# Performance work log

Measured on AMD Instinct MI355X. Metric: run time of the kernel, lower is better.

Reference implementation:

```python
import jax, jax.numpy as jnp
import numpy as np

# Module config (from init_kwargs): Occ3D-nuScenes volume
VOL_MIN = np.array([-40.0, -40.0, -1.0], dtype=np.float32)
VOXEL_SIZE = 0.4
GRID_SHAPE = (200, 200, 16)  # (vol_max - vol_min) / voxel_size
K = 6          # fixed per-gaussian window; covers radii <= 0.6m (bbox span <= 5 voxels)
N_GAUSS = 32768
N_DIMS = 16


def setup_inputs() -> dict:
    key = jax.random.key(0)
    k1, k2, k3, k4, k5 = jax.random.split(key, 5)
    # Means strictly inside the volume with 1m margin so bboxes stay in-grid.
    lo = jnp.array([-39.0, -39.0, 0.0], dtype=jnp.float32)
    hi = jnp.array([39.0, 39.0, 4.4], dtype=jnp.float32)
    means3d = jax.random.uniform(k1, (N_GAUSS, 3), minval=lo, maxval=hi, dtype=jnp.float32)
    # SPD covariances: Q diag(s) Q^T with eigenvalues in [0.01, 0.04]
    A = jax.random.normal(k2, (N_GAUSS, 3, 3), dtype=jnp.float32)
    Q, _ = jnp.linalg.qr(A)
    s = jax.random.uniform(k3, (N_GAUSS, 3), minval=0.01, maxval=0.04, dtype=jnp.float32)
    covs = jnp.einsum('nij,nj,nkj->nik', Q, s, Q)
    opacities = jax.random.uniform(k4, (N_GAUSS,), dtype=jnp.float32)
    features = jax.random.normal(k5, (N_GAUSS, N_DIMS), dtype=jnp.float32)
    return {"means3d": means3d, "covs": covs, "opacities": opacities, "features": features}


def reference(means3d, covs, opacities, features):
    N, D = features.shape
    dim_x, dim_y, dim_z = GRID_SHAPE
    total = dim_x * dim_y * dim_z
    vol_min = jnp.asarray(VOL_MIN)

    inv_covs = jnp.linalg.inv(covs)                                  # [N,3,3]
    radii = 3.0 * jnp.sqrt(jnp.diagonal(covs, axis1=-2, axis2=-1))   # [N,3]

    # Bounding box in voxel indices (trunc toward zero, like the triton .to(int32))
    s = (means3d - radii - vol_min) / VOXEL_SIZE
    e = (means3d + radii - vol_min) / VOXEL_SIZE
    start = jnp.maximum(0, s.astype(jnp.int32))                      # [N,3]
    end = jnp.minimum(jnp.array(GRID_SHAPE, jnp.int32), e.astype(jnp.int32) + 1)

    offs = jnp.arange(K, dtype=jnp.int32)
    ix = start[:, 0:1] + offs   # [N,K]
    iy = start[:, 1:2] + offs
    iz = start[:, 2:3] + offs
    mask = ((ix < end[:, 0:1])[:, :, None, None]
            & (iy < end[:, 1:2])[:, None, :, None]
            & (iz < end[:, 2:3])[:, None, None, :])                  # [N,K,K,K]

    # Voxel-corner minus mean offsets (matches kernel: x*vs + vol_min - m)
    px = ix.astype(means3d.dtype) * VOXEL_SIZE + vol_min[0] - means3d[:, 0:1]  # [N,K]
    py = iy.astype(means3d.dtype) * VOXEL_SIZE + vol_min[1] - means3d[:, 1:2]
    pz = iz.astype(means3d.dtype) * VOXEL_SIZE + vol_min[2] - means3d[:, 2:3]
    d = jnp.stack(jnp.broadcast_arrays(px[:, :, None, None],
                                       py[:, None, :, None],
                                       pz[:, None, None, :]), axis=-1)  # [N,K,K,K,3]

    mahal = jnp.einsum('nxyzi,nij,nxyzj->nxyz', d, inv_covs, d)      # [N,K,K,K]
    density = opacities[:, None, None, None] * jnp.exp(-0.5 * mahal)
    density = jnp.where(mask, density, 0.0)

    flat_idx = (ix[:, :, None, None] * (dim_y * dim_z)
                + iy[:, None, :, None] * dim_z
                + iz[:, None, None, :])                               # [N,K,K,K]
    idx = flat_idx.reshape(-1)

    grid_density = jnp.zeros((total,), density.dtype).at[idx].add(density.reshape(-1))

    contrib = density[..., None] * features[:, None, None, None, :]   # [N,K,K,K,D]
    grid_feats = jnp.zeros((total, D), density.dtype).at[:, -1].set(1e-5)
    grid_feats = grid_feats.at[idx].add(contrib.reshape(-1, D))
    grid_feats = grid_feats / jnp.clip(grid_density, 1e-6, None)[:, None]

    return grid_density.reshape(GRID_SHAPE), grid_feats.reshape(*GRID_SHAPE, D)
```

## Files before the change

### kernel.cpp

```cpp
#include <hip/hip_runtime.h>
#include <math.h>

constexpr int   GX = 200, GY = 200, GZ = 16;
constexpr int   TOTAL = GX * GY * GZ;
constexpr int   ND = 16;
constexpr int   KW = 6;
constexpr float VS = 0.4f;
constexpr float VMINX = -40.0f, VMINY = -40.0f, VMINZ = -1.0f;

constexpr int   TS = 4;
constexpr int   TX = 50, TY = 50, TZ = 4;
constexpr int   NT = TX * TY * TZ;
constexpr int   RS = 20;
constexpr int   CAP = 128;
constexpr int   BR  = 12;
constexpr float NHL2E = -0.72134752044448170f;


__device__ __forceinline__ unsigned bf16_rne(float x) {
    unsigned u = __float_as_uint(x);
    return (u + 0x7fffu + ((u >> 16) & 1u)) >> 16;
}

__global__ __launch_bounds__(256) void gv_prep(
    const float* __restrict__ means, const float* __restrict__ covs,
    const float* __restrict__ opac,  const float* __restrict__ feats,
    float* __restrict__ gdata, int* __restrict__ counts,
    int* __restrict__ entries, int n)
{
    int g = blockIdx.x * 256 + threadIdx.x;
    if (g >= n) return;
    const float* cv = covs + (size_t)g * 9;
    float a = cv[0], b = cv[1], c = cv[2], d = cv[4], e = cv[5], f = cv[8];
    float A = d * f - e * e;
    float B = c * e - b * f;
    float C = b * e - c * d;
    float invdet = 1.0f / (a * A + b * B + c * C);
    float mx = means[g * 3 + 0], my = means[g * 3 + 1], mz = means[g * 3 + 2];
    float rx = 3.0f * sqrtf(a), ry = 3.0f * sqrtf(d), rz = 3.0f * sqrtf(f);
    int sx = max(0, (int)((mx - rx - VMINX) / VS));
    int sy = max(0, (int)((my - ry - VMINY) / VS));
    int sz = max(0, (int)((mz - rz - VMINZ) / VS));
    int ex = min(GX, (int)((mx + rx - VMINX) / VS) + 1); ex = min(ex, sx + KW);
    int ey = min(GY, (int)((my + ry - VMINY) / VS) + 1); ey = min(ey, sy + KW);
    int ez = min(GZ, (int)((mz + rz - VMINZ) / VS) + 1); ez = min(ez, sz + KW);

    float rec[RS];
    rec[0] = mx; rec[1] = my; rec[2] = mz; rec[3] = opac[g];
    rec[4] = (A * invdet) * NHL2E;
    rec[5] = (B * invdet) * (2.0f * NHL2E);
    rec[6] = (C * invdet) * (2.0f * NHL2E);
    rec[7] = ((a * f - c * c) * invdet) * NHL2E;
    rec[8] = ((b * c - a * e) * invdet) * (2.0f * NHL2E);
    rec[9] = ((a * d - b * b) * invdet) * NHL2E;
    rec[10] = __int_as_float(sx | (sy << 8) | (sz << 16));
    rec[11] = __int_as_float(ex | (ey << 8) | (ez << 16));
    const float* fr = feats + (size_t)g * ND;
#pragma unroll
    for (int q = 0; q < 8; ++q) {
        unsigned lo = bf16_rne(fr[2 * q]);
        unsigned hi = bf16_rne(fr[2 * q + 1]);
        rec[12 + q] = __uint_as_float(lo | (hi << 16));
    }
    float4* dst = (float4*)(gdata + (size_t)g * RS);
#pragma unroll
    for (int q = 0; q < 5; ++q) dst[q] = ((const float4*)rec)[q];

    int tx0 = sx >> 2, tx1 = (ex - 1) >> 2;
    int ty0 = sy >> 2, ty1 = (ey - 1) >> 2;
    int tz0 = sz >> 2, tz1 = (ez - 1) >> 2;
    for (int tx = tx0; tx <= tx1; ++tx)
        for (int ty = ty0; ty <= ty1; ++ty)
            for (int tz = tz0; tz <= tz1; ++tz) {
                int tile = (tx * TY + ty) * TZ + tz;
                int slot = atomicAdd(&counts[tile], 1);
                if (slot < CAP) entries[(size_t)tile * CAP + slot] = g;
            }
}

__global__ __launch_bounds__(256) void gv_tile(
    const float* __restrict__ gdata, const int* __restrict__ counts,
    const int* __restrict__ entries, float* __restrict__ out)
{
    const int wv   = threadIdx.x >> 6;
    const int lane = threadIdx.x & 63;
    const int p    = blockIdx.x * 4 + wv;
    const int tz   = p % TZ;
    const int ty   = (p / TZ) % TY;
    const int tx   = p / (TZ * TY);

    __shared__ float sbuf[4][2][BR * RS];

    const int lz = lane & 3, ly = (lane >> 2) & 3, lx = lane >> 4;
    const int ix = tx * TS + lx, iy = ty * TS + ly, iz = tz * TS + lz;
    const float pxc = (float)ix * VS + VMINX;
    const float pyc = (float)iy * VS + VMINY;
    const float pzc = (float)iz * VS + VMINZ;

    float accd = 0.0f;
    float accf[ND];
#pragma unroll
    for (int c = 0; c < ND; ++c) accf[c] = 0.0f;
    accf[ND - 1] = 1e-5f;

    const int cnt = __builtin_amdgcn_readfirstlane(min(counts[p], CAP));
    const int* __restrict__ el = entries + (size_t)p * CAP;

    const int  rl = lane / 5;
    const int  fc = lane - rl * 5;
    const bool stager = lane < 60;
    const int  wslot = rl * RS + fc * 4;

    if (cnt > 0) {
        const int nb = (cnt + BR - 1) / BR;
        float* b0 = &sbuf[wv][0][0];
        float* b1 = &sbuf[wv][1][0];

        float4 vn; int idn2 = 0;
        if (stager) {
            int id0 = el[min(rl, cnt - 1)];
            float4 v0 = *(const float4*)(gdata + (size_t)id0 * RS + fc * 4);
            *(float4*)(b0 + wslot) = v0;
            int idn = el[min(BR + rl, cnt - 1)];
            vn = *(const float4*)(gdata + (size_t)idn * RS + fc * 4);
            idn2 = el[min(2 * BR + rl, cnt - 1)];
        }

        for (int b = 0; b < nb; ++b) {
            if (b + 1 < nb && stager) {
                float* dstb = ((b + 1) & 1) ? b1 : b0;
                *(float4*)(dstb + wslot) = vn;
                vn = *(const float4*)(gdata + (size_t)idn2 * RS + fc * 4);
                idn2 = el[min((b + 3) * BR + rl, cnt - 1)];
            }
            const float* rb = (b & 1) ? b1 : b0;
            const int rn = min(BR, cnt - b * BR);
            for (int r = 0; r < rn; ++r) {
                const float* rec = rb + r * RS;
                float4 c2 = *(const float4*)(rec + 8);
                int spk = __float_as_int(c2.z), epk = __float_as_int(c2.w);
                int sx = spk & 255, sy = (spk >> 8) & 255, sz = (spk >> 16) & 255;
                int ex = epk & 255, ey = (epk >> 8) & 255, ez = (epk >> 16) & 255;
                bool in = (ix >= sx) & (ix < ex)
                        & (iy >= sy) & (iy < ey)
                        & (iz >= sz) & (iz < ez);

                float4 c0 = *(const float4*)(rec);
                float4 c1 = *(const float4*)(rec + 4);
                float px = pxc - c0.x;
                float py = pyc - c0.y;
                float pz = pzc - c0.z;
                float q = c1.x * px * px + c1.w * py * py + c2.y * pz * pz
                        + c1.y * px * py + c1.z * px * pz + c2.x * py * pz;
                float dens = c0.w * __builtin_amdgcn_exp2f(q);
                dens = in ? dens : 0.0f;
                accd += dens;

                uint4 fA = *(const uint4*)(rec + 12);
                uint4 fB = *(const uint4*)(rec + 16);
#define BFLO(u) __uint_as_float((u) << 16)
#define BFHI(u) __uint_as_float((u) & 0xffff0000u)
                accf[0]  = fmaf(dens, BFLO(fA.x), accf[0]);
                accf[1]  = fmaf(dens, BFHI(fA.x), accf[1]);
                accf[2]  = fmaf(dens, BFLO(fA.y), accf[2]);
                accf[3]  = fmaf(dens, BFHI(fA.y), accf[3]);
                accf[4]  = fmaf(dens, BFLO(fA.z), accf[4]);
                accf[5]  = fmaf(dens, BFHI(fA.z), accf[5]);
                accf[6]  = fmaf(dens, BFLO(fA.w), accf[6]);
                accf[7]  = fmaf(dens, BFHI(fA.w), accf[7]);
                accf[8]  = fmaf(dens, BFLO(fB.x), accf[8]);
                accf[9]  = fmaf(dens, BFHI(fB.x), accf[9]);
                accf[10] = fmaf(dens, BFLO(fB.y), accf[10]);
                accf[11] = fmaf(dens, BFHI(fB.y), accf[11]);
                accf[12] = fmaf(dens, BFLO(fB.z), accf[12]);
                accf[13] = fmaf(dens, BFHI(fB.z), accf[13]);
                accf[14] = fmaf(dens, BFLO(fB.w), accf[14]);
                accf[15] = fmaf(dens, BFHI(fB.w), accf[15]);
#undef BFLO
#undef BFHI
            }
        }
    }

    const int flat = (ix * GY + iy) * GZ + iz;
    out[flat] = accd;
    float inv = 1.0f / fmaxf(accd, 1e-6f);
    float4* fo = (float4*)(out + TOTAL + (size_t)flat * ND);
#pragma unroll
    for (int q = 0; q < 4; ++q) {
        float4 w;
        w.x = accf[q * 4 + 0] * inv;
        w.y = accf[q * 4 + 1] * inv;
        w.z = accf[q * 4 + 2] * inv;
        w.w = accf[q * 4 + 3] * inv;
        fo[q] = w;
    }
}

extern "C" void kernel_launch(void* const* d_in, const int* in_sizes, int n_in,
                              void* d_out, int out_size, void* d_ws, size_t ws_size,
                              hipStream_t stream) {
    const float* means = (const float*)d_in[0];
    const float* covs  = (const float*)d_in[1];
    const float* opac  = (const float*)d_in[2];
    const float* feats = (const float*)d_in[3];
    float* out = (float*)d_out;
    const int n = in_sizes[2];

    float* gdata   = (float*)d_ws;
    int*   counts  = (int*)(gdata + (size_t)n * RS);
    int*   entries = counts + ((NT + 63) & ~63);

    hipMemsetAsync(counts, 0, NT * sizeof(int), stream);
    gv_prep<<<(n + 255) / 256, 256, 0, stream>>>(means, covs, opac, feats,
                                                 gdata, counts, entries, n);
    gv_tile<<<NT / 4, 256, 0, stream>>>(gdata, counts, entries, out);
}
```

Before: 106.4 us.

## Compact gaussian record to 64 bytes and drop counts memset

```diff
diff --git a/kernel.cpp b/kernel.cpp
--- a/kernel.cpp
+++ b/kernel.cpp
@@ -1,4 +1,5 @@
 #include <hip/hip_runtime.h>
+#include <hip/hip_fp16.h>
 #include <math.h>
 
 constexpr int   GX = 200, GY = 200, GZ = 16;
@@ -11,22 +12,31 @@
 constexpr int   TS = 4;
 constexpr int   TX = 50, TY = 50, TZ = 4;
 constexpr int   NT = TX * TY * TZ;
-constexpr int   RS = 20;
+constexpr int   RS = 16;
 constexpr int   CAP = 128;
-constexpr int   BR  = 12;
+constexpr int   BR  = 16;
 constexpr float NHL2E = -0.72134752044448170f;
 
+
+__device__ int g_counts[NT];
 
 __device__ __forceinline__ unsigned bf16_rne(float x) {
     unsigned u = __float_as_uint(x);
     return (u + 0x7fffu + ((u >> 16) & 1u)) >> 16;
 }
+__device__ __forceinline__ float pk2bf(float a, float b) {
+    return __uint_as_float(bf16_rne(a) | (bf16_rne(b) << 16));
+}
+__device__ __forceinline__ float pk2h(float a, float b) {
+    unsigned ua = __half_as_ushort(__float2half_rn(a));
+    unsigned ub = __half_as_ushort(__float2half_rn(b));
+    return __uint_as_float(ua | (ub << 16));
+}
 
 __global__ __launch_bounds__(256) void gv_prep(
     const float* __restrict__ means, const float* __restrict__ covs,
     const float* __restrict__ opac,  const float* __restrict__ feats,
-    float* __restrict__ gdata, int* __restrict__ counts,
-    int* __restrict__ entries, int n)
+    float* __restrict__ gdata, int* __restrict__ entries, int n)
 {
     int g = blockIdx.x * 256 + threadIdx.x;
     if (g >= n) return;
@@ -45,26 +55,27 @@
     int ey = min(GY, (int)((my + ry - VMINY) / VS) + 1); ey = min(ey, sy + KW);
     int ez = min(GZ, (int)((mz + rz - VMINZ) / VS) + 1); ez = min(ez, sz + KW);
 
+    float q00 = (A * invdet) * NHL2E;
+    float q01 = (B * invdet) * (2.0f * NHL2E);
+    float q02 = (C * invdet) * (2.0f * NHL2E);
+    float q11 = ((a * f - c * c) * invdet) * NHL2E;
+    float q12 = ((b * c - a * e) * invdet) * (2.0f * NHL2E);
+    float q22 = ((a * d - b * b) * invdet) * NHL2E;
+
     float rec[RS];
     rec[0] = mx; rec[1] = my; rec[2] = mz; rec[3] = opac[g];
-    rec[4] = (A * invdet) * NHL2E;
-    rec[5] = (B * invdet) * (2.0f * NHL2E);
-    rec[6] = (C * invdet) * (2.0f * NHL2E);
-    rec[7] = ((a * f - c * c) * invdet) * NHL2E;
-    rec[8] = ((b * c - a * e) * invdet) * (2.0f * NHL2E);
-    rec[9] = ((a * d - b * b) * invdet) * NHL2E;
-    rec[10] = __int_as_float(sx | (sy << 8) | (sz << 16));
-    rec[11] = __int_as_float(ex | (ey << 8) | (ez << 16));
+    rec[4] = pk2h(q00, q01);
+    rec[5] = pk2h(q02, q11);
+    rec[6] = pk2h(q12, q22);
+    rec[7] = __int_as_float(sx | (sy << 8) | (sz << 16)
+                          | ((ex - sx) << 21) | ((ey - sy) << 24) | ((ez - sz) << 27));
     const float* fr = feats + (size_t)g * ND;
 #pragma unroll
-    for (int q = 0; q < 8; ++q) {
-        unsigned lo = bf16_rne(fr[2 * q]);
-        unsigned hi = bf16_rne(fr[2 * q + 1]);
-        rec[12 + q] = __uint_as_float(lo | (hi << 16));
-    }
+    for (int q = 0; q < 8; ++q)
+        rec[8 + q] = pk2bf(fr[2 * q], fr[2 * q + 1]);
     float4* dst = (float4*)(gdata + (size_t)g * RS);
 #pragma unroll
-    for (int q = 0; q < 5; ++q) dst[q] = ((const float4*)rec)[q];
+    for (int q = 0; q < 4; ++q) dst[q] = ((const float4*)rec)[q];
 
     int tx0 = sx >> 2, tx1 = (ex - 1) >> 2;
     int ty0 = sy >> 2, ty1 = (ey - 1) >> 2;
@@ -73,14 +84,14 @@
         for (int ty = ty0; ty <= ty1; ++ty)
             for (int tz = tz0; tz <= tz1; ++tz) {
                 int tile = (tx * TY + ty) * TZ + tz;
-                int slot = atomicAdd(&counts[tile], 1);
+                int slot = atomicAdd(&g_counts[tile], 1);
                 if (slot < CAP) entries[(size_t)tile * CAP + slot] = g;
             }
 }
 
 __global__ __launch_bounds__(256) void gv_tile(
-    const float* __restrict__ gdata, const int* __restrict__ counts,
-    const int* __restrict__ entries, float* __restrict__ out)
+    const float* __restrict__ gdata, const int* __restrict__ entries,
+    float* __restrict__ out)
 {
     const int wv   = threadIdx.x >> 6;
     const int lane = threadIdx.x & 63;
@@ -103,31 +114,27 @@
     for (int c = 0; c < ND; ++c) accf[c] = 0.0f;
     accf[ND - 1] = 1e-5f;
 
-    const int cnt = __builtin_amdgcn_readfirstlane(min(counts[p], CAP));
+    const int cnt = __builtin_amdgcn_readfirstlane(min(g_counts[p], CAP));
     const int* __restrict__ el = entries + (size_t)p * CAP;
 
-    const int  rl = lane / 5;
-    const int  fc = lane - rl * 5;
-    const bool stager = lane < 60;
-    const int  wslot = rl * RS + fc * 4;
+    const int rl = lane >> 2;
+    const int fc = lane & 3;
+    const int wslot = rl * RS + fc * 4;
 
     if (cnt > 0) {
-        const int nb = (cnt + BR - 1) / BR;
+        const int nb = (cnt + BR - 1) >> 4;
         float* b0 = &sbuf[wv][0][0];
         float* b1 = &sbuf[wv][1][0];
 
-        float4 vn; int idn2 = 0;
-        if (stager) {
-            int id0 = el[min(rl, cnt - 1)];
-            float4 v0 = *(const float4*)(gdata + (size_t)id0 * RS + fc * 4);
-            *(float4*)(b0 + wslot) = v0;
-            int idn = el[min(BR + rl, cnt - 1)];
-            vn = *(const float4*)(gdata + (size_t)idn * RS + fc * 4);
-            idn2 = el[min(2 * BR + rl, cnt - 1)];
-        }
+        int id0 = el[min(rl, cnt - 1)];
+        float4 v0 = *(const float4*)(gdata + (size_t)id0 * RS + fc * 4);
+        *(float4*)(b0 + wslot) = v0;
+        int idn = el[min(BR + rl, cnt - 1)];
+        float4 vn = *(const float4*)(gdata + (size_t)idn * RS + fc * 4);
+        int idn2 = el[min(2 * BR + rl, cnt - 1)];
 
         for (int b = 0; b < nb; ++b) {
-            if (b + 1 < nb && stager) {
+            if (b + 1 < nb) {
                 float* dstb = ((b + 1) & 1) ? b1 : b0;
                 *(float4*)(dstb + wslot) = vn;
                 vn = *(const float4*)(gdata + (size_t)idn2 * RS + fc * 4);
@@ -137,29 +144,36 @@
             const int rn = min(BR, cnt - b * BR);
             for (int r = 0; r < rn; ++r) {
                 const float* rec = rb + r * RS;
-                float4 c2 = *(const float4*)(rec + 8);
-                int spk = __float_as_int(c2.z), epk = __float_as_int(c2.w);
-                int sx = spk & 255, sy = (spk >> 8) & 255, sz = (spk >> 16) & 255;
-                int ex = epk & 255, ey = (epk >> 8) & 255, ez = (epk >> 16) & 255;
+#define BFLO(u) __uint_as_float((u) << 16)
+#define BFHI(u) __uint_as_float((u) & 0xffff0000u)
+                float4 c1 = *(const float4*)(rec + 4);
+                unsigned bpk = __float_as_uint(c1.w);
+                int sx = bpk & 255, sy = (bpk >> 8) & 255, sz = (bpk >> 16) & 31;
+                int ex = sx + ((bpk >> 21) & 7);
+                int ey = sy + ((bpk >> 24) & 7);
+                int ez = sz + ((bpk >> 27) & 7);
                 bool in = (ix >= sx) & (ix < ex)
                         & (iy >= sy) & (iy < ey)
                         & (iz >= sz) & (iz < ez);
 
                 float4 c0 = *(const float4*)(rec);
-                float4 c1 = *(const float4*)(rec + 4);
+                __half2 hA = *(const __half2*)&c1.x;
+                __half2 hB = *(const __half2*)&c1.y;
+                __half2 hC = *(const __half2*)&c1.z;
+                float q00 = __low2float(hA), q01 = __high2float(hA);
+                float q02 = __low2float(hB), q11 = __high2float(hB);
+                float q12 = __low2float(hC), q22 = __high2float(hC);
                 float px = pxc - c0.x;
                 float py = pyc - c0.y;
                 float pz = pzc - c0.z;
-                float q = c1.x * px * px + c1.w * py * py + c2.y * pz * pz
-                        + c1.y * px * py + c1.z * px * pz + c2.x * py * pz;
+                float q = q00 * px * px + q11 * py * py + q22 * pz * pz
+                        + q01 * px * py + q02 * px * pz + q12 * py * pz;
                 float dens = c0.w * __builtin_amdgcn_exp2f(q);
                 dens = in ? dens : 0.0f;
                 accd += dens;
 
-                uint4 fA = *(const uint4*)(rec + 12);
-                uint4 fB = *(const uint4*)(rec + 16);
-#define BFLO(u) __uint_as_float((u) << 16)
-#define BFHI(u) __uint_as_float((u) & 0xffff0000u)
+                uint4 fA = *(const uint4*)(rec + 8);
+                uint4 fB = *(const uint4*)(rec + 12);
                 accf[0]  = fmaf(dens, BFLO(fA.x), accf[0]);
                 accf[1]  = fmaf(dens, BFHI(fA.x), accf[1]);
                 accf[2]  = fmaf(dens, BFLO(fA.y), accf[2]);
@@ -195,6 +209,8 @@
         w.w = accf[q * 4 + 3] * inv;
         fo[q] = w;
     }
+
+    if (lane == 0) g_counts[p] = 0;
 }
 
 extern "C" void kernel_launch(void* const* d_in, const int* in_sizes, int n_in,
@@ -208,11 +224,9 @@
     const int n = in_sizes[2];
 
     float* gdata   = (float*)d_ws;
-    int*   counts  = (int*)(gdata + (size_t)n * RS);
-    int*   entries = counts + ((NT + 63) & ~63);
-
-    hipMemsetAsync(counts, 0, NT * sizeof(int), stream);
+    int*   entries = (int*)(gdata + (size_t)n * RS);
+
     gv_prep<<<(n + 255) / 256, 256, 0, stream>>>(means, covs, opac, feats,
-                                                 gdata, counts, entries, n);
-    gv_tile<<<NT / 4, 256, 0, stream>>>(gdata, counts, entries, out);
-}
+                                                 gdata, entries, n);
+    gv_tile<<<NT / 4, 256, 0, stream>>>(gdata, entries, out);
+}
```

Result: no change. 106.4 us (+0.0%).
